# Kernel tuning notes

Measured on AMD Instinct MI355X. Metric: run time of the kernel, lower is better.

The kernel has to match this reference:

```python
import jax, jax.numpy as jnp
import numpy as np

D_MODEL = 1024
N_HEADS = 16
D_K = D_MODEL // N_HEADS


def setup_inputs() -> dict:
    key = jax.random.key(0)
    ks = jax.random.split(key, 12)
    B, S, D, H = 2, 2048, D_MODEL, N_HEADS
    s = 1.0 / np.sqrt(D)
    inp = {
        "x": jax.random.normal(ks[0], (B, S, D), jnp.float32),
        "Wq": jax.random.normal(ks[1], (D, D), jnp.float32) * s,
        "bq": jnp.zeros((D,), jnp.float32),
        "Wk": jax.random.normal(ks[2], (D, D), jnp.float32) * s,
        "bk": jnp.zeros((D,), jnp.float32),
        "Wv": jax.random.normal(ks[3], (D, D), jnp.float32) * s,
        "bv": jnp.zeros((D,), jnp.float32),
        "Wo": jax.random.normal(ks[4], (D, D), jnp.float32) * s,
        "bo": jnp.zeros((D,), jnp.float32),
        "Wp": jax.random.normal(ks[5], (D, H), jnp.float32) * s,
        "bp": jnp.zeros((H,), jnp.float32),
        "alpha": jax.random.normal(ks[6], (H,), jnp.float32) * 0.1,
    }
    return inp


def reference(x, Wq, bq, Wk, bk, Wv, bv, Wo, bo, Wp, bp, alpha):
    B, S, D = x.shape
    H, dk = N_HEADS, D_K
    scale = dk ** -0.5
    # projections -> (B, H, S, dk)
    Q = (x @ Wq + bq).reshape(B, S, H, dk).transpose(0, 2, 1, 3)
    K = (x @ Wk + bk).reshape(B, S, H, dk).transpose(0, 2, 1, 3)
    V = (x @ Wv + bv).reshape(B, S, H, dk).transpose(0, 2, 1, 3)
    scores = jnp.einsum("bhid,bhjd->bhij", Q, K) * scale  # (B,H,S,S)
    # phase derived from x: (B,S,H) -> (B,H,S)
    phase = (x @ Wp + bp).transpose(0, 2, 1)
    # coherence(i,j) = cos(phi_i - phi_j), per batch/head
    coherence = jnp.cos(phase[:, :, :, None] - phase[:, :, None, :])
    scores = scores + alpha[None, :, None, None] * coherence
    attn = jax.nn.softmax(scores, axis=-1)
    out = jnp.einsum("bhij,bhjd->bhid", attn, V)  # (B,H,S,dk)
    out = out.transpose(0, 2, 1, 3).reshape(B, S, D)
    return out @ Wo + bo
```

## Files before the change

kernel.cpp:

```cpp
#include <hip/hip_runtime.h>
#include <math.h>


#define S_LEN 2048
#define NHEADS 16

typedef __attribute__((ext_vector_type(8))) short short8;
typedef __attribute__((ext_vector_type(4))) float floatx4;
typedef __attribute__((ext_vector_type(2))) float float2v;

__device__ inline unsigned short f2bf(float f) {
    union { float f; unsigned int i; } v; v.f = f;
    unsigned int u = v.i;
    return (unsigned short)((u + 0x7fffu + ((u >> 16) & 1u)) >> 16);
}
__device__ inline unsigned int pack2_bf16(float hi, float lo) {
    union { float f; unsigned int u; } a, b; a.f = hi; b.f = lo;
    return __builtin_amdgcn_perm(a.u, b.u, 0x07060302u);
}
__device__ inline void async_copy16(const unsigned short* src, unsigned short* dst_lds) {
    __builtin_amdgcn_global_load_lds(
        (const __attribute__((address_space(1))) unsigned int*)(src),
        (__attribute__((address_space(3))) unsigned int*)(dst_lds), 16, 0, 0);
}
__device__ inline void async_copy4(const float* src, float* dst_lds) {
    __builtin_amdgcn_global_load_lds(
        (const __attribute__((address_space(1))) unsigned int*)(src),
        (__attribute__((address_space(3))) unsigned int*)(dst_lds), 4, 0, 0);
}

__global__ __launch_bounds__(256) void prep_kernel(
    const float* __restrict__ x, const float* __restrict__ Wp,
    const float* __restrict__ bp,
    const float* __restrict__ w0, const float* __restrict__ w1,
    const float* __restrict__ w2, const float* __restrict__ w3,
    unsigned short* __restrict__ d0, unsigned short* __restrict__ d1,
    unsigned short* __restrict__ d2, unsigned short* __restrict__ d3,
    float* __restrict__ cosP, float* __restrict__ sinP,
    unsigned short* __restrict__ xb) {
    __shared__ __align__(16) unsigned short shmem[64 * 72];
    int t = threadIdx.x;
    if (blockIdx.x < 4096) {
        float* fb = reinterpret_cast<float*>(shmem);
        float* xs = fb;
        float4* red4 = reinterpret_cast<float4*>(fb + 1024);
        int bid = blockIdx.x;
        int b = bid >> 11, s = bid & 2047;
        const float* xr = x + (size_t)bid * 1024;
        float4 xv = *reinterpret_cast<const float4*>(&xr[t * 4]);
        {
            uint2 o;
            o.x = (unsigned int)f2bf(xv.x) | ((unsigned int)f2bf(xv.y) << 16);
            o.y = (unsigned int)f2bf(xv.z) | ((unsigned int)f2bf(xv.w) << 16);
            *reinterpret_cast<uint2*>(&xb[(size_t)bid * 1024 + t * 4]) = o;
        }
        *reinterpret_cast<float4*>(&xs[t * 4]) = xv;
        __syncthreads();
        float f0 = 0.f, f1 = 0.f, f2 = 0.f, f3 = 0.f;
        int krow = t >> 2;
        const float4* wp4 = reinterpret_cast<const float4*>(Wp);
#pragma unroll
        for (int i = 0; i < 16; i++) {
            float4 wv = wp4[i * 256 + t];
            float xk = xs[i * 64 + krow];
            f0 += xk * wv.x; f1 += xk * wv.y; f2 += xk * wv.z; f3 += xk * wv.w;
        }
        red4[t] = make_float4(f0, f1, f2, f3);
        __syncthreads();
        if (t < 16) {
            int b2 = t >> 2, comp = t & 3;
            const float* rf = fb + 1024;
            float sum = bp[t];
#pragma unroll
            for (int j = 0; j < 64; j++) sum += rf[(4 * j + b2) * 4 + comp];
            float sv, cv;
            __sincosf(sum, &sv, &cv);
            size_t o = ((size_t)b * NHEADS + t) * S_LEN + s;
            cosP[o] = cv; sinP[o] = sv;
        }
    } else {
        unsigned short (*tile)[72] = reinterpret_cast<unsigned short (*)[72]>(shmem);
        int bid = blockIdx.x - 4096;
        int mat = bid >> 8;
        int tl  = bid & 255;
        int tr = tl >> 4, tc = tl & 15;
        const float* src    = (mat == 0) ? w0 : (mat == 1) ? w1 : (mat == 2) ? w2 : w3;
        unsigned short* dst = (mat == 0) ? d0 : (mat == 1) ? d1 : (mat == 2) ? d2 : d3;
        int col = t & 63, rbase = (t >> 6) * 16;
#pragma unroll
        for (int i = 0; i < 16; i++) {
            int row = rbase + i;
            tile[row][col] = f2bf(src[(size_t)(tr * 64 + row) * 1024 + tc * 64 + col]);
        }
        __syncthreads();
#pragma unroll
        for (int i = 0; i < 16; i++) {
            int row = rbase + i;
            dst[(size_t)(tc * 64 + row) * 1024 + tr * 64 + col] = tile[col][row];
        }
    }
}

template <int MT>
__global__ __launch_bounds__(256) void gemm_bt(
    const unsigned short* __restrict__ A, const unsigned short* __restrict__ BT,
    int N, int mode,
    const float* __restrict__ b0, const float* __restrict__ b1,
    const float* __restrict__ b2,
    unsigned short* __restrict__ o0, unsigned short* __restrict__ o1,
    unsigned short* __restrict__ o2, float* __restrict__ of) {
    __shared__ __align__(16) unsigned short As[MT * 32];
    __shared__ __align__(16) unsigned short Bs[128 * 32];
    const int K = 1024;
    const int MI = MT / 32;
    int t = threadIdx.x;
    int mBase = blockIdx.x * MT;
    int nBase = blockIdx.y * 128;
    int w = t >> 6, lane = t & 63, l15 = lane & 15, quad = lane >> 4;
    int wm = (w & 1) * (MT / 2), wn = (w >> 1) * 64;
    floatx4 acc[MI][4];
#pragma unroll
    for (int i = 0; i < MI; i++)
#pragma unroll
        for (int j = 0; j < 4; j++) acc[i][j] = (floatx4){0.f, 0.f, 0.f, 0.f};

    int arow = t >> 2, aseg = (t & 3) * 8;
    for (int k0 = 0; k0 < K; k0 += 32) {
        __syncthreads();
#pragma unroll
        for (int i = 0; i < MT / 64; i++)
            async_copy16(&A[(size_t)(mBase + i * 64 + arow) * K + k0 + aseg],
                         &As[(i * 64 + arow) * 32 + aseg]);
#pragma unroll
        for (int i = 0; i < 2; i++)
            async_copy16(&BT[(size_t)(nBase + i * 64 + arow) * K + k0 + aseg],
                         &Bs[(i * 64 + arow) * 32 + aseg]);
        __syncthreads();
        short8 af[MI], bfr[4];
#pragma unroll
        for (int mi = 0; mi < MI; mi++)
            af[mi] = *reinterpret_cast<const short8*>(&As[(wm + mi * 16 + l15) * 32 + quad * 8]);
#pragma unroll
        for (int ni = 0; ni < 4; ni++)
            bfr[ni] = *reinterpret_cast<const short8*>(&Bs[(wn + ni * 16 + l15) * 32 + quad * 8]);
#pragma unroll
        for (int mi = 0; mi < MI; mi++)
#pragma unroll
            for (int ni = 0; ni < 4; ni++)
                acc[mi][ni] = __builtin_amdgcn_mfma_f32_16x16x32_bf16(af[mi], bfr[ni], acc[mi][ni], 0, 0, 0);
    }

#pragma unroll
    for (int mi = 0; mi < MI; mi++) {
        int rowB = mBase + wm + mi * 16 + quad * 4;
#pragma unroll
        for (int ni = 0; ni < 4; ni++) {
            int col = nBase + wn + ni * 16 + l15;
            if (mode == 0) {
                float bias = b0[col];
#pragma unroll
                for (int r = 0; r < 4; r++) {
                    of[(size_t)(rowB + r) * N + col] = acc[mi][ni][r] + bias;
                }
            } else {
                int mat = col >> 10, nn = col & 1023;
                int h = nn >> 6, d = nn & 63;
                int b = rowB >> 11, sidx = rowB & 2047;
                if (mat == 2) {
                    float bv = b2[nn];
                    int jj = sidx & 63;
                    size_t rowOff = ((size_t)((b * NHEADS + h) * 64 + d)) * S_LEN +
                                    (sidx & ~63);
#pragma unroll
                    for (int r = 0; r < 4; r++) {
                        int j2 = jj + r;
                        int jt = j2 >> 4;
                        int u = (jt >> 1) * 32 + ((j2 & 15) >> 2) * 8 + (jt & 1) * 4 + (j2 & 3);
                        o2[rowOff + u] = f2bf(acc[mi][ni][r] + bv);
                    }
                } else {
                    const float* bias  = (mat == 0) ? b0 : b1;
                    unsigned short* op = (mat == 0) ? o0 : o1;
                    float bv = bias[nn];
                    float scl = (mat == 0) ? 0.18033688f : 1.0f;
#pragma unroll
                    for (int r = 0; r < 4; r++) {
                        float cv = (acc[mi][ni][r] + bv) * scl;
                        op[(((size_t)b * NHEADS + h) * S_LEN + (sidx + r)) * 64 + d] = f2bf(cv);
                    }
                }
            }
        }
    }
}

__global__ __launch_bounds__(1024) void attn_kernel(
    const unsigned short* __restrict__ Qg, const unsigned short* __restrict__ Kg,
    const unsigned short* __restrict__ VTg,
    const float* __restrict__ cosP, const float* __restrict__ sinP,
    const float* __restrict__ alpha, unsigned short* __restrict__ ctx) {
    __shared__ __align__(16) unsigned short KsB[4][64 * 64];
    __shared__ __align__(16) unsigned short VtB[4][64 * 64];
    __shared__ __align__(16) float csB[4][128];

    int x = blockIdx.x;
    int bh = (x & 7) * 4 + (x >> 6);
    int qt = (x >> 3) & 7;
    int t = threadIdx.x, w = t >> 6, lane = t & 63, l15 = lane & 15, quad = lane >> 4;
    int m0 = qt * 256 + w * 16;
    size_t base = (size_t)bh * (S_LEN * 64);
    size_t phBase = (size_t)bh * S_LEN;
    const float L2E = 1.44269504f;

    int th = t & 511;
    int sj = th >> 3, sg = th & 7;
    int srot = ((sg - (sj & 7)) & 7) * 8;
    bool stK = (t < 512);

    short8 qf[2];
#pragma unroll
    for (int c = 0; c < 2; c++)
        qf[c] = *reinterpret_cast<const short8*>(
            &Qg[base + (size_t)(m0 + l15) * 64 + c * 32 + quad * 8]);

    float alph = alpha[bh & 15] * L2E;
    float ci = alph * cosP[phBase + m0 + l15];
    float si = alph * sinP[phBase + m0 + l15];
    float2v ci2 = (float2v){ci, ci}, si2 = (float2v){si, si};

    {
#pragma unroll
        for (int t0 = 0; t0 < 2; t0++) {
            if (stK) async_copy16(&Kg[base + (size_t)(t0 * 64 + sj) * 64 + srot], &KsB[t0][th * 8]);
            else     async_copy16(&VTg[base + (size_t)sj * S_LEN + t0 * 64 + srot], &VtB[t0][th * 8]);
            if (w == 4)      async_copy4(&cosP[phBase + t0 * 64 + lane], &csB[t0][lane]);
            else if (w == 5) async_copy4(&sinP[phBase + t0 * 64 + lane], &csB[t0][64 + lane]);
        }
    }

    floatx4 oacc[4], lacc;
#pragma unroll
    for (int tt = 0; tt < 4; tt++) oacc[tt] = (floatx4){0.f, 0.f, 0.f, 0.f};
    lacc = (floatx4){0.f, 0.f, 0.f, 0.f};
    const short8 ones8 = {(short)0x3F80, (short)0x3F80, (short)0x3F80, (short)0x3F80,
                          (short)0x3F80, (short)0x3F80, (short)0x3F80, (short)0x3F80};

    int rot = l15 & 7;
    int cb0 = 16 * ((quad + rot) & 7);
    int cb1 = 16 * ((quad + 4 + rot) & 7);

    for (int kt = 0; kt < 32; kt++) {
        int p = kt & 3;
        if ((kt & 1) == 0) {
            __syncthreads();
#pragma unroll
            for (int d = 2; d <= 3; d++) {
                int kn = kt + d;
                if (kn < 32) {
                    int pn = kn & 3;
                    if (stK) async_copy16(&Kg[base + (size_t)(kn * 64 + sj) * 64 + srot], &KsB[pn][th * 8]);
                    else     async_copy16(&VTg[base + (size_t)sj * S_LEN + kn * 64 + srot], &VtB[pn][th * 8]);
                    if (w == 4)      async_copy4(&cosP[phBase + kn * 64 + lane], &csB[pn][lane]);
                    else if (w == 5) async_copy4(&sinP[phBase + kn * 64 + lane], &csB[pn][64 + lane]);
                }
            }
        }

        floatx4 st[4];
        __builtin_amdgcn_s_setprio(1);
#pragma unroll
        for (int jt = 0; jt < 4; jt++) {
            const char* kr = (const char*)&KsB[p][(jt * 16 + l15) * 64];
            short8 kf0 = *reinterpret_cast<const short8*>(kr + cb0);
            short8 kf1 = *reinterpret_cast<const short8*>(kr + cb1);
            floatx4 s = (floatx4){0.f, 0.f, 0.f, 0.f};
            s = __builtin_amdgcn_mfma_f32_16x16x32_bf16(kf0, qf[0], s, 0, 0, 0);
            s = __builtin_amdgcn_mfma_f32_16x16x32_bf16(kf1, qf[1], s, 0, 0, 0);
            st[jt] = s;
        }
        __builtin_amdgcn_s_setprio(0);

        union PW { unsigned int u[4]; short8 s8; };
        PW P0, P1;
#pragma unroll
        for (int jt = 0; jt < 4; jt++) {
            float4 cj4 = *reinterpret_cast<const float4*>(&csB[p][jt * 16 + quad * 4]);
            float4 sj4 = *reinterpret_cast<const float4*>(&csB[p][64 + jt * 16 + quad * 4]);
            float2v st01 = (float2v){st[jt][0], st[jt][1]};
            float2v st23 = (float2v){st[jt][2], st[jt][3]};
            float2v c01 = (float2v){cj4.x, cj4.y}, c23 = (float2v){cj4.z, cj4.w};
            float2v s01 = (float2v){sj4.x, sj4.y}, s23 = (float2v){sj4.z, sj4.w};
            float2v a01 = si2 * s01 + (ci2 * c01 + st01);
            float2v a23 = si2 * s23 + (ci2 * c23 + st23);
            unsigned int wA = pack2_bf16(__builtin_amdgcn_exp2f(a01.y),
                                         __builtin_amdgcn_exp2f(a01.x));
            unsigned int wB = pack2_bf16(__builtin_amdgcn_exp2f(a23.y),
                                         __builtin_amdgcn_exp2f(a23.x));
            if (jt == 0)      { P0.u[0] = wA; P0.u[1] = wB; }
            else if (jt == 1) { P0.u[2] = wA; P0.u[3] = wB; }
            else if (jt == 2) { P1.u[0] = wA; P1.u[1] = wB; }
            else              { P1.u[2] = wA; P1.u[3] = wB; }
        }

        __builtin_amdgcn_s_setprio(1);
#pragma unroll
        for (int c = 0; c < 2; c++) {
            short8 pf = c ? P1.s8 : P0.s8;
            int cb = c ? cb1 : cb0;
#pragma unroll
            for (int tt = 0; tt < 4; tt++) {
                const char* vr = (const char*)&VtB[p][(tt * 16 + l15) * 64];
                short8 vf = *reinterpret_cast<const short8*>(vr + cb);
                oacc[tt] = __builtin_amdgcn_mfma_f32_16x16x32_bf16(pf, vf, oacc[tt], 0, 0, 0);
            }
            lacc = __builtin_amdgcn_mfma_f32_16x16x32_bf16(pf, ones8, lacc, 0, 0, 0);
        }
        __builtin_amdgcn_s_setprio(0);
    }

    int b = bh >> 4, h = bh & 15;
    float inv[4];
#pragma unroll
    for (int r = 0; r < 4; r++) inv[r] = 1.0f / lacc[r];
#pragma unroll
    for (int tt = 0; tt < 4; tt++)
#pragma unroll
        for (int r = 0; r < 4; r++) {
            int srow = m0 + quad * 4 + r;
            ctx[((size_t)(b * S_LEN + srow)) * 1024 + h * 64 + tt * 16 + l15] =
                f2bf(oacc[tt][r] * inv[r]);
        }
}

extern "C" void kernel_launch(void* const* d_in, const int* in_sizes, int n_in,
                              void* d_out, int out_size, void* d_ws, size_t ws_size,
                              hipStream_t stream) {
    const float* x     = (const float*)d_in[0];
    const float* Wq    = (const float*)d_in[1];
    const float* bq    = (const float*)d_in[2];
    const float* Wk    = (const float*)d_in[3];
    const float* bk    = (const float*)d_in[4];
    const float* Wv    = (const float*)d_in[5];
    const float* bv    = (const float*)d_in[6];
    const float* Wo    = (const float*)d_in[7];
    const float* bo    = (const float*)d_in[8];
    const float* Wp    = (const float*)d_in[9];
    const float* bp    = (const float*)d_in[10];
    const float* alpha = (const float*)d_in[11];
    float* out = (float*)d_out;

    const size_t MB = 1048576;
    char* ws = (char*)d_ws;
    unsigned short* WT   = (unsigned short*)(ws);
    unsigned short* WoT  = (unsigned short*)(ws + 6 * MB);
    unsigned short* xb   = (unsigned short*)(ws + 8 * MB);
    unsigned short* ctx  = (unsigned short*)(ws + 8 * MB);
    unsigned short* Qw   = (unsigned short*)(ws + 16 * MB);
    unsigned short* Kw   = (unsigned short*)(ws + 24 * MB);
    unsigned short* VTg  = (unsigned short*)(ws + 32 * MB);
    float* cosP          = (float*)(ws + 40 * MB);
    float* sinP          = (float*)(ws + 40 * MB + 262144);

    prep_kernel<<<dim3(5120), dim3(256), 0, stream>>>(
        x, Wp, bp, Wq, Wk, Wv, Wo,
        WT, WT + 1048576, WT + 2097152, WoT, cosP, sinP, xb);
    gemm_bt<128><<<dim3(32, 24), dim3(256), 0, stream>>>(
        xb, WT, 3072, 1, bq, bk, bv, Qw, Kw, VTg, (float*)nullptr);
    attn_kernel<<<dim3(256), dim3(1024), 0, stream>>>(
        Qw, Kw, VTg, cosP, sinP, alpha, ctx);
    gemm_bt<64><<<dim3(64, 8), dim3(256), 0, stream>>>(
        ctx, WoT, 1024, 0, bo, bo, bo,
        (unsigned short*)nullptr, (unsigned short*)nullptr,
        (unsigned short*)nullptr, out);
}
```

Measured before the change: 222.2 us.

## Double-buffer LDS tiles in gemm_bt and prefetch next K-slice during MFMA

Splits the A and B shared-memory tiles into two buffers. The next K-slice is issued with async global-to-LDS copies while MFMAs run on the current slice, which removes one barrier per iteration and overlaps load latency with compute. It also raises wave priority around the MFMA block. In exchange the GEMM uses twice the LDS, which may lower occupancy.

```diff
diff --git a/kernel.cpp b/kernel.cpp
--- a/kernel.cpp
+++ b/kernel.cpp
@@ -109,8 +109,8 @@
     const float* __restrict__ b2,
     unsigned short* __restrict__ o0, unsigned short* __restrict__ o1,
     unsigned short* __restrict__ o2, float* __restrict__ of) {
-    __shared__ __align__(16) unsigned short As[MT * 32];
-    __shared__ __align__(16) unsigned short Bs[128 * 32];
+    __shared__ __align__(16) unsigned short As[2][MT * 32];
+    __shared__ __align__(16) unsigned short Bs[2][128 * 32];
     const int K = 1024;
     const int MI = MT / 32;
     int t = threadIdx.x;
@@ -125,29 +125,43 @@
         for (int j = 0; j < 4; j++) acc[i][j] = (floatx4){0.f, 0.f, 0.f, 0.f};
 
     int arow = t >> 2, aseg = (t & 3) * 8;
+#pragma unroll
+    for (int i = 0; i < MT / 64; i++)
+        async_copy16(&A[(size_t)(mBase + i * 64 + arow) * K + aseg],
+                     &As[0][(i * 64 + arow) * 32 + aseg]);
+#pragma unroll
+    for (int i = 0; i < 2; i++)
+        async_copy16(&BT[(size_t)(nBase + i * 64 + arow) * K + aseg],
+                     &Bs[0][(i * 64 + arow) * 32 + aseg]);
+
     for (int k0 = 0; k0 < K; k0 += 32) {
+        int cur = (k0 >> 5) & 1;
         __syncthreads();
-#pragma unroll
-        for (int i = 0; i < MT / 64; i++)
-            async_copy16(&A[(size_t)(mBase + i * 64 + arow) * K + k0 + aseg],
-                         &As[(i * 64 + arow) * 32 + aseg]);
-#pragma unroll
-        for (int i = 0; i < 2; i++)
-            async_copy16(&BT[(size_t)(nBase + i * 64 + arow) * K + k0 + aseg],
-                         &Bs[(i * 64 + arow) * 32 + aseg]);
-        __syncthreads();
+        if (k0 + 32 < K) {
+            int nb = cur ^ 1, kn = k0 + 32;
+#pragma unroll
+            for (int i = 0; i < MT / 64; i++)
+                async_copy16(&A[(size_t)(mBase + i * 64 + arow) * K + kn + aseg],
+                             &As[nb][(i * 64 + arow) * 32 + aseg]);
+#pragma unroll
+            for (int i = 0; i < 2; i++)
+                async_copy16(&BT[(size_t)(nBase + i * 64 + arow) * K + kn + aseg],
+                             &Bs[nb][(i * 64 + arow) * 32 + aseg]);
+        }
         short8 af[MI], bfr[4];
 #pragma unroll
         for (int mi = 0; mi < MI; mi++)
-            af[mi] = *reinterpret_cast<const short8*>(&As[(wm + mi * 16 + l15) * 32 + quad * 8]);
+            af[mi] = *reinterpret_cast<const short8*>(&As[cur][(wm + mi * 16 + l15) * 32 + quad * 8]);
 #pragma unroll
         for (int ni = 0; ni < 4; ni++)
-            bfr[ni] = *reinterpret_cast<const short8*>(&Bs[(wn + ni * 16 + l15) * 32 + quad * 8]);
+            bfr[ni] = *reinterpret_cast<const short8*>(&Bs[cur][(wn + ni * 16 + l15) * 32 + quad * 8]);
+        __builtin_amdgcn_s_setprio(1);
 #pragma unroll
         for (int mi = 0; mi < MI; mi++)
 #pragma unroll
             for (int ni = 0; ni < 4; ni++)
                 acc[mi][ni] = __builtin_amdgcn_mfma_f32_16x16x32_bf16(af[mi], bfr[ni], acc[mi][ni], 0, 0, 0);
+        __builtin_amdgcn_s_setprio(0);
     }
 
 #pragma unroll
```

New measurement: 203.5 us. -8.4%, faster.
